# Performance work log

Measured on AMD Instinct MI355X. Metric: run time of the kernel, lower is better.

The kernel has to match this reference:

```python
import jax, jax.numpy as jnp
import numpy as np

# ---- module hyperparameters (mirror NDP defaults / init_kwargs) ----
ACTION_DIM = 16
NUM_BASIS = 4
NUM_ACTIONS = 50
BATCH = 32768
ALPHA_P = 1.0
ALPHA_U = 10.0
BETA = 2.5
DT = 0.01                      # ode_solver_dt
STEP_DELTA = 1.0 / NUM_ACTIONS # spacing of sample_times
N_SUB = int(round(STEP_DELTA / DT))  # integrator steps per save interval (=2)

RBF_CENTERS = jnp.exp(-ALPHA_P * jnp.linspace(0.0, 1.0, NUM_BASIS))
RBF_H = NUM_BASIS / RBF_CENTERS

# Tsitouras 5(4) Butcher tableau (same as diffrax.Tsit5); fixed step so only
# the 6 interior stages + 5th-order combination are needed (FSAL k7 unused).
A21 = 0.161
A31, A32 = -0.008480655492356989, 0.335480655492357
A41, A42, A43 = 2.8971530571054935, -6.359448489975075, 4.3622954328695815
A51, A52, A53, A54 = 5.325864828439257, -11.748883564062828, 7.4955393428898365, -0.09249506636175525
A61, A62, A63, A64, A65 = 5.86145544294642, -12.92096931784711, 8.159367898576159, -0.071584973281401, -0.028269050394068383
B1, B2, B3, B4, B5, B6 = 0.09646076681806523, 0.01, 0.4798896504144996, 1.379008574103742, -3.290069515436081, 2.324710524099774


def setup_inputs() -> dict:
    key = jax.random.key(0)
    k1, k2, k3 = jax.random.split(key, 3)
    return {
        "init_u_udot": 0.1 * jax.random.normal(k1, (BATCH, 2 * ACTION_DIM), jnp.float32),
        "rbf_weights": jax.random.normal(k2, (BATCH, ACTION_DIM * NUM_BASIS), jnp.float32),
        "goals": jax.random.normal(k3, (BATCH, ACTION_DIM), jnp.float32),
    }


def _ndp_flow(init_u_udot, rbf_weights, goals):
    """Batched fixed-step Tsit5 solve of the NDP ODE; returns u at sample_times."""
    B, A = init_u_udot.shape[0], ACTION_DIM
    u0s = init_u_udot[:, :A]
    W = rbf_weights.reshape(B, A, NUM_BASIS)
    gmu0 = goals - u0s                                      # (B, A), constant forcing scale
    y0 = jnp.concatenate([init_u_udot, jnp.ones((B, 1), init_u_udot.dtype)], axis=1)  # (B, 2A+1)

    def f(y):  # autonomous vector field, vectorized over batch
        u, ud, p = y[:, :A], y[:, A:2 * A], y[:, 2 * A:]    # p: (B,1)
        psi = jnp.exp(-RBF_H * (p - RBF_CENTERS) ** 2)      # (B, K)
        force = (jnp.einsum('bak,bk->ba', W, psi)
                 / jnp.sum(psi, axis=1, keepdims=True)) * p * gmu0
        udd = ALPHA_U * (BETA * (goals - u) - ud) + force
        return jnp.concatenate([ud, udd, -ALPHA_P * p], axis=1)

    h = DT

    def step(y, _):
        k1 = f(y)
        k2 = f(y + h * A21 * k1)
        k3 = f(y + h * (A31 * k1 + A32 * k2))
        k4 = f(y + h * (A41 * k1 + A42 * k2 + A43 * k3))
        k5 = f(y + h * (A51 * k1 + A52 * k2 + A53 * k3 + A54 * k4))
        k6 = f(y + h * (A61 * k1 + A62 * k2 + A63 * k3 + A64 * k4 + A65 * k5))
        yn = y + h * (B1 * k1 + B2 * k2 + B3 * k3 + B4 * k4 + B5 * k5 + B6 * k6)
        return yn, yn

    n_steps = (NUM_ACTIONS - 1) * N_SUB
    _, ys = jax.lax.scan(step, y0, None, length=n_steps)    # (steps, B, 2A+1)
    # sample_times[0] = 0 -> y0; later samples land exactly on every N_SUB-th step
    saved = jnp.concatenate([y0[None], ys[N_SUB - 1::N_SUB]], axis=0)  # (N, B, 2A+1)
    return jnp.transpose(saved[:, :, :A], (1, 0, 2))        # (B, N, A)


def reference(init_u_udot, rbf_weights, goals):
    return _ndp_flow(init_u_udot, rbf_weights, goals)
```

## Files before the change

kernel.cpp:

```cpp
#include <hip/hip_runtime.h>
#include <math.h>

#define DH   0.01
#define CA21 0.161
#define CA31 (-0.008480655492356989)
#define CA32 0.335480655492357
#define CA41 2.8971530571054935
#define CA42 (-6.359448489975075)
#define CA43 4.3622954328695815
#define CA51 5.325864828439257
#define CA52 (-11.748883564062828)
#define CA53 7.4955393428898365
#define CA54 (-0.09249506636175525)
#define CA61 5.86145544294642
#define CA62 (-12.92096931784711)
#define CA63 8.159367898576159
#define CA64 (-0.071584973281401)
#define CA65 (-0.028269050394068383)
#define CB1  0.09646076681806523
#define CB2  0.01
#define CB3  0.4798896504144996
#define CB4  1.379008574103742
#define CB5  (-3.290069515436081)
#define CB6  2.324710524099774

__device__ __forceinline__ void rk_probe(double yu, double yd, const double F[6],
                                         double& ou, double& od) {
    const double h = DH;
    double k1u = yd;
    double k1d = -25.0*yu - 10.0*yd + F[0];
    double tu, td;
    tu = yu + h*(CA21*k1u); td = yd + h*(CA21*k1d);
    double k2u = td, k2d = -25.0*tu - 10.0*td + F[1];
    tu = yu + h*(CA31*k1u + CA32*k2u); td = yd + h*(CA31*k1d + CA32*k2d);
    double k3u = td, k3d = -25.0*tu - 10.0*td + F[2];
    tu = yu + h*(CA41*k1u + CA42*k2u + CA43*k3u);
    td = yd + h*(CA41*k1d + CA42*k2d + CA43*k3d);
    double k4u = td, k4d = -25.0*tu - 10.0*td + F[3];
    tu = yu + h*(CA51*k1u + CA52*k2u + CA53*k3u + CA54*k4u);
    td = yd + h*(CA51*k1d + CA52*k2d + CA53*k3d + CA54*k4d);
    double k5u = td, k5d = -25.0*tu - 10.0*td + F[4];
    tu = yu + h*(CA61*k1u + CA62*k2u + CA63*k3u + CA64*k4u + CA65*k5u);
    td = yd + h*(CA61*k1d + CA62*k2d + CA63*k3d + CA64*k4d + CA65*k5d);
    double k6u = td, k6d = -25.0*tu - 10.0*td + F[5];
    ou = yu + h*(CB1*k1u + CB2*k2u + CB3*k3u + CB4*k4u + CB5*k5u + CB6*k6u);
    od = yd + h*(CB1*k1d + CB2*k2d + CB3*k3d + CB4*k4d + CB5*k5d + CB6*k6d);
}

__global__ void ndp_setup(float* __restrict__ ws) {
    int t = threadIdx.x;

    double vu[6], vd[6];
    {
        double F[6];
        #pragma unroll
        for (int i = 0; i < 6; ++i) {
            #pragma unroll
            for (int j = 0; j < 6; ++j) F[j] = 0.0;
            F[i] = 1.0;
            rk_probe(0.0, 0.0, F, vu[i], vd[i]);
        }
    }
    double Fz[6] = {0,0,0,0,0,0};
    double m00, m10, m01, m11;
    rk_probe(1.0, 0.0, Fz, m00, m10);
    rk_probe(0.0, 1.0, Fz, m01, m11);

    const double h = DH;
    double gam[6];
    double k1 = -1.0; gam[0] = 1.0;
    gam[1] = 1.0 + h*CA21*k1;                          double k2 = -gam[1];
    gam[2] = 1.0 + h*(CA31*k1 + CA32*k2);              double k3 = -gam[2];
    gam[3] = 1.0 + h*(CA41*k1 + CA42*k2 + CA43*k3);    double k4 = -gam[3];
    gam[4] = 1.0 + h*(CA51*k1 + CA52*k2 + CA53*k3 + CA54*k4);          double k5 = -gam[4];
    gam[5] = 1.0 + h*(CA61*k1 + CA62*k2 + CA63*k3 + CA64*k4 + CA65*k5); double k6 = -gam[5];
    double r = 1.0 + h*(CB1*k1 + CB2*k2 + CB3*k3 + CB4*k4 + CB5*k5 + CB6*k6);

    double C[4], H[4];
    #pragma unroll
    for (int k = 0; k < 4; ++k) { C[k] = exp(-(double)k / 3.0); H[k] = 4.0 / C[k]; }

    if (t < 49) {
        double qu[2][4], qd[2][4];
        #pragma unroll
        for (int s = 0; s < 2; ++s)
            #pragma unroll
            for (int k = 0; k < 4; ++k) { qu[s][k] = 0.0; qd[s][k] = 0.0; }

        double pbase = pow(r, (double)(2 * t));
        #pragma unroll
        for (int sub = 0; sub < 2; ++sub) {
            double pb = sub ? pbase * r : pbase;
            #pragma unroll
            for (int i = 0; i < 6; ++i) {
                double pi = gam[i] * pb;
                double ps[4], ssum = 0.0;
                #pragma unroll
                for (int k = 0; k < 4; ++k) {
                    double d0 = pi - C[k];
                    ps[k] = exp(-H[k] * d0 * d0);
                    ssum += ps[k];
                }
                double sc = pi / ssum;
                #pragma unroll
                for (int k = 0; k < 4; ++k) {
                    double sk = ps[k] * sc;
                    qu[sub][k] += vu[i] * sk;
                    qd[sub][k] += vd[i] * sk;
                }
            }
        }
        #pragma unroll
        for (int k = 0; k < 4; ++k) {
            double Qu = m00*qu[0][k] + m01*qd[0][k] + qu[1][k];
            double Qd = m10*qu[0][k] + m11*qd[0][k] + qd[1][k];
            ws[8 + t*8 + k]     = (float)Qu;
            ws[8 + t*8 + 4 + k] = (float)Qd;
        }
    }
    if (t == 49) {
        double gvu = 0.0, gvd = 0.0;
        #pragma unroll
        for (int i = 0; i < 6; ++i) { gvu += vu[i]; gvd += vd[i]; }
        gvu *= 25.0; gvd *= 25.0;
        ws[0] = (float)(m00*m00 + m01*m10);
        ws[1] = (float)(m00*m01 + m01*m11);
        ws[2] = (float)(m10*m00 + m11*m10);
        ws[3] = (float)(m10*m01 + m11*m11);
        ws[4] = (float)((m00 + 1.0)*gvu + m01*gvd);
        ws[5] = (float)(m10*gvu + (m11 + 1.0)*gvd);
        ws[6] = 0.0f; ws[7] = 0.0f;
    }
}

__global__ __launch_bounds__(256) void ndp_main(
    const float* __restrict__ init,
    const float* __restrict__ rbfw,
    const float* __restrict__ goals,
    const float* __restrict__ cst,
    float* __restrict__ out) {
    int tid = blockIdx.x * blockDim.x + threadIdx.x;
    int b = tid >> 4;
    int a = tid & 15;

    float u  = init[b * 32 + a];
    float ud = init[b * 32 + 16 + a];
    float g  = goals[b * 16 + a];
    float gmu = g - u;

    float4 w = *reinterpret_cast<const float4*>(&rbfw[b * 64 + a * 4]);
    float W0 = gmu * w.x, W1 = gmu * w.y, W2 = gmu * w.z, W3 = gmu * w.w;

    float m00 = cst[0], m01 = cst[1], m10 = cst[2], m11 = cst[3];
    float gcu = g * cst[4], gcd = g * cst[5];

    float* op = out + (size_t)b * 800 + a;
    *op = u;
    const float* q = cst + 8;

    #pragma unroll 7
    for (int m = 0; m < 49; ++m) {
        float4 qu = *reinterpret_cast<const float4*>(q + m * 8);
        float4 qd = *reinterpret_cast<const float4*>(q + m * 8 + 4);
        float fu = gcu + W0*qu.x + W1*qu.y + W2*qu.z + W3*qu.w;
        float fd = gcd + W0*qd.x + W1*qd.y + W2*qd.z + W3*qd.w;
        float un  = m00*u + m01*ud + fu;
        float udn = m10*u + m11*ud + fd;
        u = un; ud = udn;
        op[(m + 1) * 16] = u;
    }
}

extern "C" void kernel_launch(void* const* d_in, const int* in_sizes, int n_in,
                              void* d_out, int out_size, void* d_ws, size_t ws_size,
                              hipStream_t stream) {
    const float* init  = (const float*)d_in[0];
    const float* rbfw  = (const float*)d_in[1];
    const float* goals = (const float*)d_in[2];
    float* out = (float*)d_out;
    float* ws  = (float*)d_ws;

    ndp_setup<<<1, 64, 0, stream>>>(ws);

    const int total = 32768 * 16;
    ndp_main<<<total / 256, 256, 0, stream>>>(init, rbfw, goals, ws, out);
}
```

Before: 29.95 us.

## Precompute closed-form coefficient table at compile time, parallelize output rows

Builds the full 50-row affine coefficient table with constexpr evaluation and places it in __constant__ memory, so the per-call setup kernel launch goes away. Each output sample becomes a direct linear combination of u0, ud0, g and the scaled weights, which removes the sequential recurrence. The 50 rows are then split across 4 lane groups per batch element, and outputs use nontemporal stores. The coefficients depend only on fixed hyperparameters, not on the inputs, so this is legitimate constant folding. It adds float rounding differences from the reformulation.

```diff
diff --git a/kernel.cpp b/kernel.cpp
--- a/kernel.cpp
+++ b/kernel.cpp
@@ -1,173 +1,153 @@
 #include <hip/hip_runtime.h>
-#include <math.h>
 
-#define DH   0.01
-#define CA21 0.161
-#define CA31 (-0.008480655492356989)
-#define CA32 0.335480655492357
-#define CA41 2.8971530571054935
-#define CA42 (-6.359448489975075)
-#define CA43 4.3622954328695815
-#define CA51 5.325864828439257
-#define CA52 (-11.748883564062828)
-#define CA53 7.4955393428898365
-#define CA54 (-0.09249506636175525)
-#define CA61 5.86145544294642
-#define CA62 (-12.92096931784711)
-#define CA63 8.159367898576159
-#define CA64 (-0.071584973281401)
-#define CA65 (-0.028269050394068383)
-#define CB1  0.09646076681806523
-#define CB2  0.01
-#define CB3  0.4798896504144996
-#define CB4  1.379008574103742
-#define CB5  (-3.290069515436081)
-#define CB6  2.324710524099774
+namespace ct {
 
-__device__ __forceinline__ void rk_probe(double yu, double yd, const double F[6],
-                                         double& ou, double& od) {
-    const double h = DH;
-    double k1u = yd;
-    double k1d = -25.0*yu - 10.0*yd + F[0];
-    double tu, td;
-    tu = yu + h*(CA21*k1u); td = yd + h*(CA21*k1d);
-    double k2u = td, k2d = -25.0*tu - 10.0*td + F[1];
-    tu = yu + h*(CA31*k1u + CA32*k2u); td = yd + h*(CA31*k1d + CA32*k2d);
-    double k3u = td, k3d = -25.0*tu - 10.0*td + F[2];
-    tu = yu + h*(CA41*k1u + CA42*k2u + CA43*k3u);
-    td = yd + h*(CA41*k1d + CA42*k2d + CA43*k3d);
-    double k4u = td, k4d = -25.0*tu - 10.0*td + F[3];
-    tu = yu + h*(CA51*k1u + CA52*k2u + CA53*k3u + CA54*k4u);
-    td = yd + h*(CA51*k1d + CA52*k2d + CA53*k3d + CA54*k4d);
-    double k5u = td, k5d = -25.0*tu - 10.0*td + F[4];
-    tu = yu + h*(CA61*k1u + CA62*k2u + CA63*k3u + CA64*k4u + CA65*k5u);
-    td = yd + h*(CA61*k1d + CA62*k2d + CA63*k3d + CA64*k4d + CA65*k5d);
-    double k6u = td, k6d = -25.0*tu - 10.0*td + F[5];
-    ou = yu + h*(CB1*k1u + CB2*k2u + CB3*k3u + CB4*k4u + CB5*k5u + CB6*k6u);
-    od = yd + h*(CB1*k1d + CB2*k2d + CB3*k3d + CB4*k4d + CB5*k5d + CB6*k6d);
+constexpr double H   = 0.01;
+constexpr double A21 = 0.161;
+constexpr double A31 = -0.008480655492356989, A32 = 0.335480655492357;
+constexpr double A41 = 2.8971530571054935,  A42 = -6.359448489975075, A43 = 4.3622954328695815;
+constexpr double A51 = 5.325864828439257,   A52 = -11.748883564062828, A53 = 7.4955393428898365, A54 = -0.09249506636175525;
+constexpr double A61 = 5.86145544294642,    A62 = -12.92096931784711,  A63 = 8.159367898576159,  A64 = -0.071584973281401, A65 = -0.028269050394068383;
+constexpr double B1 = 0.09646076681806523,  B2 = 0.01, B3 = 0.4798896504144996, B4 = 1.379008574103742, B5 = -3.290069515436081, B6 = 2.324710524099774;
+
+constexpr double cexp(double x) {
+    const double LN2 = 0.69314718055994530942;
+    double t = x / LN2;
+    int n = (int)(t >= 0.0 ? t + 0.5 : t - 0.5);
+    double r = x - (double)n * LN2;
+    double sum = 1.0, term = 1.0;
+    for (int i = 1; i < 26; ++i) { term *= r / (double)i; sum += term; }
+    if (n >= 0) { for (int i = 0; i <  n; ++i) sum *= 2.0; }
+    else        { for (int i = 0; i < -n; ++i) sum *= 0.5; }
+    return sum;
 }
 
-__global__ void ndp_setup(float* __restrict__ ws) {
-    int t = threadIdx.x;
+struct Pair { double u, d; };
 
-    double vu[6], vd[6];
-    {
-        double F[6];
-        #pragma unroll
+constexpr Pair rk(double yu, double yd, const double* F) {
+    double k1u = yd, k1d = -25.0*yu - 10.0*yd + F[0];
+    double tu = yu + H*(A21*k1u), td = yd + H*(A21*k1d);
+    double k2u = td, k2d = -25.0*tu - 10.0*td + F[1];
+    tu = yu + H*(A31*k1u + A32*k2u); td = yd + H*(A31*k1d + A32*k2d);
+    double k3u = td, k3d = -25.0*tu - 10.0*td + F[2];
+    tu = yu + H*(A41*k1u + A42*k2u + A43*k3u);
+    td = yd + H*(A41*k1d + A42*k2d + A43*k3d);
+    double k4u = td, k4d = -25.0*tu - 10.0*td + F[3];
+    tu = yu + H*(A51*k1u + A52*k2u + A53*k3u + A54*k4u);
+    td = yd + H*(A51*k1d + A52*k2d + A53*k3d + A54*k4d);
+    double k5u = td, k5d = -25.0*tu - 10.0*td + F[4];
+    tu = yu + H*(A61*k1u + A62*k2u + A63*k3u + A64*k4u + A65*k5u);
+    td = yd + H*(A61*k1d + A62*k2d + A63*k3d + A64*k4d + A65*k5d);
+    double k6u = td, k6d = -25.0*tu - 10.0*td + F[5];
+    double ou = yu + H*(B1*k1u + B2*k2u + B3*k3u + B4*k4u + B5*k5u + B6*k6u);
+    double od = yd + H*(B1*k1d + B2*k2d + B3*k3d + B4*k4d + B5*k5d + B6*k6d);
+    return {ou, od};
+}
+
+struct CoefTab { float c[50][8]; };
+
+constexpr CoefTab make_coefs() {
+    CoefTab T{};
+    double vu[6] = {}, vd[6] = {};
+    for (int i = 0; i < 6; ++i) {
+        double F[6] = {0,0,0,0,0,0};
+        F[i] = 1.0;
+        Pair pr = rk(0.0, 0.0, F);
+        vu[i] = pr.u; vd[i] = pr.d;
+    }
+    double Fz[6] = {0,0,0,0,0,0};
+    Pair mc0 = rk(1.0, 0.0, Fz);
+    Pair mc1 = rk(0.0, 1.0, Fz);
+    double m00 = mc0.u, m10 = mc0.d, m01 = mc1.u, m11 = mc1.d;
+
+    double gam[6] = {};
+    double k1 = -1.0; gam[0] = 1.0;
+    gam[1] = 1.0 + H*A21*k1;                                            double k2 = -gam[1];
+    gam[2] = 1.0 + H*(A31*k1 + A32*k2);                                 double k3 = -gam[2];
+    gam[3] = 1.0 + H*(A41*k1 + A42*k2 + A43*k3);                        double k4 = -gam[3];
+    gam[4] = 1.0 + H*(A51*k1 + A52*k2 + A53*k3 + A54*k4);               double k5 = -gam[4];
+    gam[5] = 1.0 + H*(A61*k1 + A62*k2 + A63*k3 + A64*k4 + A65*k5);      double k6 = -gam[5];
+    double r = 1.0 + H*(B1*k1 + B2*k2 + B3*k3 + B4*k4 + B5*k5 + B6*k6);
+
+    double C[4] = {}, Hh[4] = {};
+    for (int k = 0; k < 4; ++k) { C[k] = cexp(-(double)k / 3.0); Hh[k] = 4.0 / C[k]; }
+
+    double gvu = 0.0, gvd = 0.0;
+    for (int i = 0; i < 6; ++i) { gvu += vu[i]; gvd += vd[i]; }
+    gvu *= 25.0; gvd *= 25.0;
+
+    double Su[7] = {1,0,0,0,0,0,0};
+    double Sd[7] = {0,1,0,0,0,0,0};
+    for (int j = 0; j < 7; ++j) T.c[0][j] = (float)Su[j];
+    T.c[0][7] = 0.0f;
+
+    double p = 1.0;
+    int save = 1;
+    for (int n = 0; n < 98; ++n) {
+        double Qu[4] = {}, Qd[4] = {};
         for (int i = 0; i < 6; ++i) {
-            #pragma unroll
-            for (int j = 0; j < 6; ++j) F[j] = 0.0;
-            F[i] = 1.0;
-            rk_probe(0.0, 0.0, F, vu[i], vd[i]);
+            double pi = gam[i] * p;
+            double ps[4] = {}; double ss = 0.0;
+            for (int k = 0; k < 4; ++k) {
+                double d0 = pi - C[k];
+                ps[k] = cexp(-Hh[k] * d0 * d0);
+                ss += ps[k];
+            }
+            double sc = pi / ss;
+            for (int k = 0; k < 4; ++k) {
+                double sk = ps[k] * sc;
+                Qu[k] += vu[i] * sk;
+                Qd[k] += vd[i] * sk;
+            }
+        }
+        double nu[7] = {}, nd[7] = {};
+        for (int j = 0; j < 7; ++j) {
+            nu[j] = m00*Su[j] + m01*Sd[j];
+            nd[j] = m10*Su[j] + m11*Sd[j];
+        }
+        nu[2] += gvu; nd[2] += gvd;
+        for (int k = 0; k < 4; ++k) { nu[3+k] += Qu[k]; nd[3+k] += Qd[k]; }
+        for (int j = 0; j < 7; ++j) { Su[j] = nu[j]; Sd[j] = nd[j]; }
+        p *= r;
+        if (n & 1) {
+            for (int j = 0; j < 7; ++j) T.c[save][j] = (float)Su[j];
+            T.c[save][7] = 0.0f;
+            ++save;
         }
     }
-    double Fz[6] = {0,0,0,0,0,0};
-    double m00, m10, m01, m11;
-    rk_probe(1.0, 0.0, Fz, m00, m10);
-    rk_probe(0.0, 1.0, Fz, m01, m11);
+    return T;
+}
 
-    const double h = DH;
-    double gam[6];
-    double k1 = -1.0; gam[0] = 1.0;
-    gam[1] = 1.0 + h*CA21*k1;                          double k2 = -gam[1];
-    gam[2] = 1.0 + h*(CA31*k1 + CA32*k2);              double k3 = -gam[2];
-    gam[3] = 1.0 + h*(CA41*k1 + CA42*k2 + CA43*k3);    double k4 = -gam[3];
-    gam[4] = 1.0 + h*(CA51*k1 + CA52*k2 + CA53*k3 + CA54*k4);          double k5 = -gam[4];
-    gam[5] = 1.0 + h*(CA61*k1 + CA62*k2 + CA63*k3 + CA64*k4 + CA65*k5); double k6 = -gam[5];
-    double r = 1.0 + h*(CB1*k1 + CB2*k2 + CB3*k3 + CB4*k4 + CB5*k5 + CB6*k6);
+}
 
-    double C[4], H[4];
-    #pragma unroll
-    for (int k = 0; k < 4; ++k) { C[k] = exp(-(double)k / 3.0); H[k] = 4.0 / C[k]; }
-
-    if (t < 49) {
-        double qu[2][4], qd[2][4];
-        #pragma unroll
-        for (int s = 0; s < 2; ++s)
-            #pragma unroll
-            for (int k = 0; k < 4; ++k) { qu[s][k] = 0.0; qd[s][k] = 0.0; }
-
-        double pbase = pow(r, (double)(2 * t));
-        #pragma unroll
-        for (int sub = 0; sub < 2; ++sub) {
-            double pb = sub ? pbase * r : pbase;
-            #pragma unroll
-            for (int i = 0; i < 6; ++i) {
-                double pi = gam[i] * pb;
-                double ps[4], ssum = 0.0;
-                #pragma unroll
-                for (int k = 0; k < 4; ++k) {
-                    double d0 = pi - C[k];
-                    ps[k] = exp(-H[k] * d0 * d0);
-                    ssum += ps[k];
-                }
-                double sc = pi / ssum;
-                #pragma unroll
-                for (int k = 0; k < 4; ++k) {
-                    double sk = ps[k] * sc;
-                    qu[sub][k] += vu[i] * sk;
-                    qd[sub][k] += vd[i] * sk;
-                }
-            }
-        }
-        #pragma unroll
-        for (int k = 0; k < 4; ++k) {
-            double Qu = m00*qu[0][k] + m01*qd[0][k] + qu[1][k];
-            double Qd = m10*qu[0][k] + m11*qd[0][k] + qd[1][k];
-            ws[8 + t*8 + k]     = (float)Qu;
-            ws[8 + t*8 + 4 + k] = (float)Qd;
-        }
-    }
-    if (t == 49) {
-        double gvu = 0.0, gvd = 0.0;
-        #pragma unroll
-        for (int i = 0; i < 6; ++i) { gvu += vu[i]; gvd += vd[i]; }
-        gvu *= 25.0; gvd *= 25.0;
-        ws[0] = (float)(m00*m00 + m01*m10);
-        ws[1] = (float)(m00*m01 + m01*m11);
-        ws[2] = (float)(m10*m00 + m11*m10);
-        ws[3] = (float)(m10*m01 + m11*m11);
-        ws[4] = (float)((m00 + 1.0)*gvu + m01*gvd);
-        ws[5] = (float)(m10*gvu + (m11 + 1.0)*gvd);
-        ws[6] = 0.0f; ws[7] = 0.0f;
-    }
-}
+constexpr ct::CoefTab h_coef = ct::make_coefs();
+__constant__ ct::CoefTab g_coef = h_coef;
 
 __global__ __launch_bounds__(256) void ndp_main(
     const float* __restrict__ init,
     const float* __restrict__ rbfw,
     const float* __restrict__ goals,
-    const float* __restrict__ cst,
     float* __restrict__ out) {
-    int tid = blockIdx.x * blockDim.x + threadIdx.x;
-    int b = tid >> 4;
-    int a = tid & 15;
+    const int lane = threadIdx.x & 63;
+    const int b    = blockIdx.x * 4 + (threadIdx.x >> 6);
+    const int rl   = lane >> 4;
+    const int a    = lane & 15;
 
-    float u  = init[b * 32 + a];
-    float ud = init[b * 32 + 16 + a];
-    float g  = goals[b * 16 + a];
-    float gmu = g - u;
-
-    float4 w = *reinterpret_cast<const float4*>(&rbfw[b * 64 + a * 4]);
-    float W0 = gmu * w.x, W1 = gmu * w.y, W2 = gmu * w.z, W3 = gmu * w.w;
-
-    float m00 = cst[0], m01 = cst[1], m10 = cst[2], m11 = cst[3];
-    float gcu = g * cst[4], gcd = g * cst[5];
+    const float u0  = init[b * 32 + a];
+    const float ud0 = init[b * 32 + 16 + a];
+    const float g   = goals[b * 16 + a];
+    const float gmu = g - u0;
+    const float4 w  = *reinterpret_cast<const float4*>(&rbfw[b * 64 + a * 4]);
+    const float p0 = gmu * w.x, p1 = gmu * w.y, p2 = gmu * w.z, p3 = gmu * w.w;
 
     float* op = out + (size_t)b * 800 + a;
-    *op = u;
-    const float* q = cst + 8;
-
-    #pragma unroll 7
-    for (int m = 0; m < 49; ++m) {
-        float4 qu = *reinterpret_cast<const float4*>(q + m * 8);
-        float4 qd = *reinterpret_cast<const float4*>(q + m * 8 + 4);
-        float fu = gcu + W0*qu.x + W1*qu.y + W2*qu.z + W3*qu.w;
-        float fd = gcd + W0*qd.x + W1*qd.y + W2*qd.z + W3*qd.w;
-        float un  = m00*u + m01*ud + fu;
-        float udn = m10*u + m11*ud + fd;
-        u = un; ud = udn;
-        op[(m + 1) * 16] = u;
+    #pragma unroll 4
+    for (int r = rl; r < 50; r += 4) {
+        const float4 c0 = *reinterpret_cast<const float4*>(&g_coef.c[r][0]);
+        const float4 c1 = *reinterpret_cast<const float4*>(&g_coef.c[r][4]);
+        const float v = c0.x*u0 + c0.y*ud0 + c0.z*g + c0.w*p0
+                      + c1.x*p1 + c1.y*p2 + c1.z*p3;
+        __builtin_nontemporal_store(v, op + r * 16);
     }
 }
 
@@ -178,10 +158,7 @@
     const float* rbfw  = (const float*)d_in[1];
     const float* goals = (const float*)d_in[2];
     float* out = (float*)d_out;
-    float* ws  = (float*)d_ws;
 
-    ndp_setup<<<1, 64, 0, stream>>>(ws);
-
-    const int total = 32768 * 16;
-    ndp_main<<<total / 256, 256, 0, stream>>>(init, rbfw, goals, ws, out);
+    const int B = in_sizes[0] / 32;
+    ndp_main<<<B / 4, 256, 0, stream>>>(init, rbfw, goals, out);
 }
```

Measured after the change: 37.94 us. 1.27x slower.
